# Optimization experiments

Measured on AMD Instinct MI355X. Metric: run time of the kernel, lower is better.

The kernel has to match this reference:

```python
import jax, jax.numpy as jnp
import numpy as np

B, N, CS, CV, K = 8, 2048, 256, 128, 3
EPS = 1e-6


def _eq_layernorm(s, v):
    # scalars: standard layernorm over channels; vectors: RMS of channel norms (equivariant)
    mu = s.mean(-1, keepdims=True)
    var = ((s - mu) ** 2).mean(-1, keepdims=True)
    s = (s - mu) * jax.lax.rsqrt(var + EPS)
    n2 = (v ** 2).sum(-1).mean(-1, keepdims=True)  # [b,n,1]
    v = v * jax.lax.rsqrt(n2 + EPS)[..., None]
    return s, v


def setup_inputs() -> dict:
    key = jax.random.key(0)
    ks = jax.random.split(key, 7)
    fan_s = K * (CS + CV)       # 1152
    fan_v = K * (CS + 2 * CV)   # 1536
    return {
        "x_s": jax.random.normal(ks[0], (B, N, CS), jnp.float32),
        "x_v": jax.random.normal(ks[1], (B, N, CV, 3), jnp.float32),
        "coords": jax.random.normal(ks[2], (B, N, 3), jnp.float32) * 10.0,
        "W_conv_s": jax.random.normal(ks[3], (fan_s, CS), jnp.float32),
        "W_conv_v": jax.random.normal(ks[4], (fan_v, CV), jnp.float32),
        "W_si_s": jax.random.normal(ks[5], (CS, CS), jnp.float32),
        "W_si_v": jax.random.normal(ks[6], (CV, CV), jnp.float32),
    }


def reference(x_s, x_v, coords, W_conv_s, W_conv_v, W_si_s, W_si_v):
    b, n, cs = x_s.shape
    cv = x_v.shape[2]
    pad = K // 2
    # 'same' padding: zeros for features, edge for coords (zero displacement at boundary)
    sp = jnp.pad(x_s, ((0, 0), (pad, pad), (0, 0)))
    vp = jnp.pad(x_v, ((0, 0), (pad, pad), (0, 0), (0, 0)))
    cp = jnp.pad(coords, ((0, 0), (pad, pad), (0, 0)), mode="edge")
    s_win = jnp.stack([sp[:, k:k + n] for k in range(K)], 2)   # [b,n,K,cs]
    v_win = jnp.stack([vp[:, k:k + n] for k in range(K)], 2)   # [b,n,K,cv,3]
    c_win = jnp.stack([cp[:, k:k + n] for k in range(K)], 2)   # [b,n,K,3]

    d = c_win - coords[:, :, None, :]
    dn = jnp.linalg.norm(d, axis=-1, keepdims=True)
    rhat = d * jnp.where(dn > 1e-6, 1.0 / jnp.maximum(dn, 1e-6), 0.0)

    # Clebsch-Gordan paths of (0e,1e) features with sh = (1, rhat)
    vdot = jnp.einsum("bnkcd,bnkd->bnkc", v_win, rhat)                    # 1x1 -> 0
    scal_in = jnp.concatenate([s_win, vdot], -1).reshape(b, n, -1)        # [b,n,K*(cs+cv)]
    s_rhat = s_win[..., None] * rhat[:, :, :, None, :]                    # 0x1 -> 1
    v_cross = jnp.cross(v_win, rhat[:, :, :, None, :])                    # 1x1 -> 1
    vec_in = jnp.concatenate([v_win, s_rhat, v_cross], 3).reshape(b, n, -1, 3)

    # SequenceConvolution linear mixing (fan-in normalized) + norm=True
    h_s = jnp.einsum("bnp,po->bno", scal_in, W_conv_s) / float(np.sqrt(scal_in.shape[-1]))
    h_v = jnp.einsum("bnpd,po->bnod", vec_in, W_conv_v) / float(np.sqrt(vec_in.shape[2]))
    h_s, h_v = _eq_layernorm(h_s, h_v)

    # SelfInteraction: per-degree channel mixing, residual=True, norm_last=True
    y_s = h_s + h_s @ W_si_s / float(np.sqrt(cs))
    y_v = h_v + jnp.einsum("bncd,co->bnod", h_v, W_si_v) / float(np.sqrt(cv))
    y_s, y_v = _eq_layernorm(y_s, y_v)

    # block Residual + final EquivariantLayerNorm
    z_s, z_v = _eq_layernorm(x_s + y_s, x_v + y_v)
    return z_s, z_v
```

## Files before the change

### kernel.cpp

```cpp
#include <hip/hip_runtime.h>
#include <hip/hip_bf16.h>


typedef __attribute__((ext_vector_type(8))) short short8;
typedef __attribute__((ext_vector_type(4))) short short4v;
typedef __attribute__((ext_vector_type(4))) float f32x4;
typedef unsigned short u16;

#define B_   8
#define N_   2048
#define EPS_ 1e-6f
#define TB   64

#define OFF_CS 0
#define OFF_V  294912
#define OFF_G  393216
#define OFF_SS 491520
#define OFF_SV 557056

#define MFMA(a,b,c) __builtin_amdgcn_mfma_f32_16x16x32_bf16((a),(b),(c),0,0,0)

__device__ __forceinline__ u16 f2b(float v){ __hip_bfloat16 h=__float2bfloat16(v); return *(u16*)&h; }

__global__ __launch_bounds__(256) void prep_weights(
    const float* __restrict__ Wcs, const float* __restrict__ Wcv,
    const float* __restrict__ Wss, const float* __restrict__ Wsv,
    u16* __restrict__ ws)
{
    const int bid = blockIdx.x;
    const float* src; int N, r0, ld, c0; u16* dst; int tile;
    if (bid < 288)      { src=Wcs; N=256; r0=0; dst=ws+OFF_CS; ld=1152; c0=0; tile=bid; }
    else if (bid < 336) { int k=(bid-288)/16; tile=(bid-288)%16;
                          src=Wcv; N=128; r0=k*512;     dst=ws+OFF_V; ld=768; c0=k*256; }
    else if (bid < 432) { int k=(bid-336)/32; tile=(bid-336)%32;
                          src=Wcv; N=128; r0=k*512+128; dst=ws+OFF_G; ld=768; c0=k*256; }
    else if (bid < 480) { int k=(bid-432)/16; tile=(bid-432)%16;
                          src=Wcv; N=128; r0=k*512+384; dst=ws+OFF_V; ld=768; c0=k*256+128; }
    else if (bid < 544) { tile=bid-480; src=Wss; N=256; r0=0; dst=ws+OFF_SS; ld=256; c0=0; }
    else                { tile=bid-544; src=Wsv; N=128; r0=0; dst=ws+OFF_SV; ld=128; c0=0; }
    const int ntN = N >> 5;
    const int kt = (tile/ntN)*32, nn = (tile%ntN)*32;
    __shared__ float t[32][33];
    const int r = threadIdx.x >> 5, c = threadIdx.x & 31;
#pragma unroll
    for (int i = 0; i < 4; ++i)
        t[r+8*i][c] = src[(size_t)(r0+kt+r+8*i)*N + nn+c];
    __syncthreads();
#pragma unroll
    for (int i = 0; i < 4; ++i)
        dst[(size_t)(nn+r+8*i)*ld + c0+kt+c] = f2b(t[c][r+8*i]);
}

__device__ __forceinline__ void ln_reduce(
    float p1[4][4], float p2[4][4], float pv[4][4], f32x4* red,
    int tid, int lm, int lq4, int w,
    float mu[4][4], float ss[4][4], float vs[4][4])
{
    __syncthreads();
#pragma unroll
    for (int m2 = 1; m2 < 16; m2 <<= 1)
#pragma unroll
        for (int m = 0; m < 4; ++m)
#pragma unroll
            for (int q = 0; q < 4; ++q) {
                p1[m][q] += __shfl_xor(p1[m][q], m2);
                p2[m][q] += __shfl_xor(p2[m][q], m2);
                pv[m][q] += __shfl_xor(pv[m][q], m2);
            }
    if (lm == 0)
#pragma unroll
        for (int m = 0; m < 4; ++m)
#pragma unroll
            for (int q = 0; q < 4; ++q) {
                f32x4 r = {p1[m][q], p2[m][q], pv[m][q], 0.f};
                red[(m*16+lq4+q)*8 + w] = r;
            }
    __syncthreads();
    if (tid < 64) {
        const int t = tid;
        f32x4 rs = red[t*8+0];
#pragma unroll
        for (int i = 1; i < 8; ++i) rs += red[t*8+i];
        const float mm = rs.x * (1.f/256.f);
        f32x4 fin;
        fin.x = mm;
        fin.y = rsqrtf(rs.y*(1.f/256.f) - mm*mm + EPS_);
        fin.z = rsqrtf(rs.z*(1.f/128.f) + EPS_);
        fin.w = 0.f;
        red[t*8 + (t&7)] = fin;
    }
    __syncthreads();
#pragma unroll
    for (int m = 0; m < 4; ++m)
#pragma unroll
        for (int q = 0; q < 4; ++q) {
            const int t = m*16 + lq4 + q;
            const f32x4 fin = red[t*8 + (t&7)];
            mu[m][q] = fin.x; ss[m][q] = fin.y; vs[m][q] = fin.z;
        }
}

__global__ __launch_bounds__(512, 2) void mixing_main(
    const float* __restrict__ x_s, const float* __restrict__ x_v,
    const float* __restrict__ coords, const u16* __restrict__ wt,
    float* __restrict__ out)
{
    __shared__ __align__(16) char smem[162816];
    u16*   fs  = (u16*)smem;
    u16*   fv  = (u16*)(smem + 50176);
    u16*   hsb = (u16*)smem;
    u16*   hvb = (u16*)(smem + 50176);
    float* xvL = (float*)(smem + 50176);
    float* rhp = (float*)(smem + 151552);
    f32x4* red = (f32x4*)(smem + 154624);

    const int tid = threadIdx.x;
    const int w   = tid >> 6, l = tid & 63;
    const int lm  = l & 15, lk8 = (l >> 4) << 3, lq4 = (l >> 4) << 2;
    const int gt0 = blockIdx.x * TB;
    const int n0  = gt0 & (N_ - 1);
    const int seq0 = gt0 - n0;
    const size_t ZV0 = (size_t)B_ * N_ * 256;

    if (tid < 192) {
        const int t = tid / 3, k = tid - 3 * (tid / 3);
        const int jn = n0 + t + k - 1;
        const int jc = jn < 0 ? 0 : (jn > N_-1 ? N_-1 : jn);
        const float* cj = coords + (size_t)(seq0 + jc) * 3;
        const float* c0p = coords + (size_t)(gt0 + t) * 3;
        const float d0 = cj[0]-c0p[0], d1 = cj[1]-c0p[1], d2 = cj[2]-c0p[2];
        const float dn = sqrtf(d0*d0 + d1*d1 + d2*d2);
        const float inv = dn > 1e-6f ? 1.f/dn : 0.f;
        rhp[(t*3+k)*4+0] = d0*inv; rhp[(t*3+k)*4+1] = d1*inv; rhp[(t*3+k)*4+2] = d2*inv;
    }
    __syncthreads();

    const f32x4 fz = {0.f,0.f,0.f,0.f};
    f32x4 acc_s[4][2];
    f32x4 accv[12];
#pragma unroll
    for (int m = 0; m < 4; ++m) { acc_s[m][0] = fz; acc_s[m][1] = fz; }
#pragma unroll
    for (int mi = 0; mi < 12; ++mi) accv[mi] = fz;

    const int bt = tid >> 3;
    const int bx = tid & 7;

#pragma unroll 1
    for (int k = 0; k < 3; ++k) {
        const int jn = n0 + bt + k - 1;
        const bool valid = (unsigned)jn < (unsigned)N_;
        const size_t j = (size_t)seq0 + (valid ? jn : 0);
        {
            const int c0 = bx * 32;
            const float4* sp = (const float4*)(x_s + j*256 + c0);
#pragma unroll
            for (int h = 0; h < 4; ++h) {
                float v[8];
                if (valid) {
                    const float4 f0 = sp[2*h], f1 = sp[2*h+1];
                    v[0]=f0.x; v[1]=f0.y; v[2]=f0.z; v[3]=f0.w;
                    v[4]=f1.x; v[5]=f1.y; v[6]=f1.z; v[7]=f1.w;
                } else {
#pragma unroll
                    for (int i = 0; i < 8; ++i) v[i] = 0.f;
                }
                short8 p;
#pragma unroll
                for (int i = 0; i < 8; ++i) p[i] = (short)f2b(v[i]);
                *(short8*)(fs + bt*392 + c0 + 8*h) = p;
            }
        }
        {
            const int ch0 = bx * 16;
            const float r0 = rhp[(bt*3+k)*4+0];
            const float r1 = rhp[(bt*3+k)*4+1];
            const float r2 = rhp[(bt*3+k)*4+2];
#pragma unroll
            for (int hh = 0; hh < 2; ++hh) {
                const int cb = ch0 + 8*hh;
                float vv[24];
                if (valid) {
                    const float4* vp = (const float4*)(x_v + ((size_t)j*128 + cb)*3);
#pragma unroll
                    for (int i = 0; i < 6; ++i) {
                        const float4 f = vp[i];
                        vv[4*i]=f.x; vv[4*i+1]=f.y; vv[4*i+2]=f.z; vv[4*i+3]=f.w;
                    }
                } else {
#pragma unroll
                    for (int i = 0; i < 24; ++i) vv[i] = 0.f;
                }
                short8 dv, w0, w1, w2, x0, x1, x2;
#pragma unroll
                for (int m = 0; m < 8; ++m) {
                    const float a0 = vv[3*m], a1 = vv[3*m+1], a2 = vv[3*m+2];
                    dv[m] = (short)f2b(a0*r0 + a1*r1 + a2*r2);
                    w0[m] = (short)f2b(a0); w1[m] = (short)f2b(a1); w2[m] = (short)f2b(a2);
                    x0[m] = (short)f2b(a1*r2 - a2*r1);
                    x1[m] = (short)f2b(a2*r0 - a0*r2);
                    x2[m] = (short)f2b(a0*r1 - a1*r0);
                }
                *(short8*)(fs + bt*392 + 256 + cb)            = dv;
                *(short8*)(fv + (0*64+bt)*264 + cb)           = w0;
                *(short8*)(fv + (1*64+bt)*264 + cb)           = w1;
                *(short8*)(fv + (2*64+bt)*264 + cb)           = w2;
                *(short8*)(fv + (0*64+bt)*264 + 128 + cb)     = x0;
                *(short8*)(fv + (1*64+bt)*264 + 128 + cb)     = x1;
                *(short8*)(fv + (2*64+bt)*264 + 128 + cb)     = x2;
            }
        }

        const u16* bS0 = wt + OFF_CS + k*384 + (size_t)((2*w+0)*16+lm)*1152;
        const u16* bS1 = wt + OFF_CS + k*384 + (size_t)((2*w+1)*16+lm)*1152;
        const u16* bGp = wt + OFF_G  + k*256 + (size_t)(w*16+lm)*768;
        const u16* bVp = wt + OFF_V  + k*256 + (size_t)(w*16+lm)*768;
        short8 Bs0[3], Bs1[3], Bg[3], Bv[4];
#pragma unroll
        for (int i = 0; i < 3; ++i) {
            Bs0[i] = *(const short8*)(bS0 + i*32 + lk8);
            Bs1[i] = *(const short8*)(bS1 + i*32 + lk8);
            Bg[i]  = *(const short8*)(bGp + i*32 + lk8);
        }
        __syncthreads();

        f32x4 agc[4] = {fz, fz, fz, fz};
#pragma unroll
        for (int ks = 0; ks < 12; ++ks) {
            const int r = ks % 3;
            const short8 b0 = Bs0[r], b1 = Bs1[r], bg = Bg[r];
            if (ks + 3 < 12) {
                Bs0[r] = *(const short8*)(bS0 + (ks+3)*32 + lk8);
                Bs1[r] = *(const short8*)(bS1 + (ks+3)*32 + lk8);
            }
            if (ks + 3 < 8)
                Bg[r] = *(const short8*)(bGp + (ks+3)*32 + lk8);
            if (ks == 9) {
#pragma unroll
                for (int i = 0; i < 4; ++i)
                    Bv[i] = *(const short8*)(bVp + i*32 + lk8);
            }
            const int ko = ks*32 + lk8;
#pragma unroll
            for (int m = 0; m < 4; ++m) {
                const short8 a = *(const short8*)(fs + (m*16+lm)*392 + ko);
                acc_s[m][0] = MFMA(a, b0, acc_s[m][0]);
                acc_s[m][1] = MFMA(a, b1, acc_s[m][1]);
                if (ks < 8) agc[m] = MFMA(a, bg, agc[m]);
            }
        }
#pragma unroll
        for (int ks = 0; ks < 8; ++ks) {
            const int r = ks & 3;
            const short8 bv = Bv[r];
            if (ks + 4 < 8)
                Bv[r] = *(const short8*)(bVp + (ks+4)*32 + lk8);
            const int ko = ks*32 + lk8;
#pragma unroll
            for (int mi = 0; mi < 12; ++mi) {
                const short8 a = *(const short8*)(
                    fv + ((mi>>2)*64 + (mi&3)*16 + lm)*264 + ko);
                accv[mi] = MFMA(a, bv, accv[mi]);
            }
        }
#pragma unroll
        for (int mi = 0; mi < 12; ++mi) {
            const int m = mi & 3, d = mi >> 2;
#pragma unroll
            for (int q = 0; q < 4; ++q)
                accv[mi][q] += agc[m][q] * rhp[((m*16+lq4+q)*3 + k)*4 + d];
        }
        __syncthreads();
    }

    const float inv_fs = 0.029462783f;
    const float inv_fv = 0.0255155136f;
#pragma unroll
    for (int m = 0; m < 4; ++m)
#pragma unroll
        for (int u = 0; u < 2; ++u)
#pragma unroll
            for (int q = 0; q < 4; ++q) acc_s[m][u][q] *= inv_fs;
#pragma unroll
    for (int mi = 0; mi < 12; ++mi)
#pragma unroll
        for (int q = 0; q < 4; ++q) accv[mi][q] *= inv_fv;

    float p1[4][4], p2[4][4], pv[4][4], mu[4][4], ss[4][4], vs[4][4];
#pragma unroll
    for (int m = 0; m < 4; ++m)
#pragma unroll
        for (int q = 0; q < 4; ++q) {
            float a = 0.f, b = 0.f, c = 0.f;
#pragma unroll
            for (int u = 0; u < 2; ++u) { const float x = acc_s[m][u][q]; a += x; b += x*x; }
#pragma unroll
            for (int d = 0; d < 3; ++d) { const float x = accv[d*4+m][q]; c += x*x; }
            p1[m][q] = a; p2[m][q] = b; pv[m][q] = c;
        }
    ln_reduce(p1, p2, pv, red, tid, lm, lq4, w, mu, ss, vs);

#pragma unroll
    for (int m = 0; m < 4; ++m)
#pragma unroll
        for (int u = 0; u < 2; ++u)
#pragma unroll
            for (int q = 0; q < 4; ++q) {
                const float h = (acc_s[m][u][q] - mu[m][q]) * ss[m][q];
                acc_s[m][u][q] = h;
                hsb[(m*16+lq4+q)*264 + (2*w+u)*16 + lm] = f2b(h);
            }
#pragma unroll
    for (int mi = 0; mi < 12; ++mi)
#pragma unroll
        for (int q = 0; q < 4; ++q) {
            const float h = accv[mi][q] * vs[mi&3][q];
            accv[mi][q] = h;
            hvb[((mi>>2)*64 + (mi&3)*16 + lq4 + q)*136 + w*16 + lm] = f2b(h);
        }

    const u16* bP0 = wt + OFF_SS + (size_t)((2*w+0)*16+lm)*256;
    const u16* bP1 = wt + OFF_SS + (size_t)((2*w+1)*16+lm)*256;
    const u16* bPv = wt + OFF_SV + (size_t)(w*16+lm)*128;
    short8 Cs0[3], Cs1[3], Cv[4];
#pragma unroll
    for (int i = 0; i < 3; ++i) {
        Cs0[i] = *(const short8*)(bP0 + i*32 + lk8);
        Cs1[i] = *(const short8*)(bP1 + i*32 + lk8);
    }
#pragma unroll
    for (int i = 0; i < 4; ++i)
        Cv[i] = *(const short8*)(bPv + i*32 + lk8);
    __syncthreads();

    f32x4 accs[4][2];
    f32x4 accw[12];
#pragma unroll
    for (int m = 0; m < 4; ++m) { accs[m][0] = fz; accs[m][1] = fz; }
#pragma unroll
    for (int mi = 0; mi < 12; ++mi) accw[mi] = fz;
#pragma unroll
    for (int ks = 0; ks < 8; ++ks) {
        const int r = ks % 3;
        const short8 c0 = Cs0[r], c1 = Cs1[r];
        if (ks + 3 < 8) {
            Cs0[r] = *(const short8*)(bP0 + (ks+3)*32 + lk8);
            Cs1[r] = *(const short8*)(bP1 + (ks+3)*32 + lk8);
        }
        const int ko = ks*32 + lk8;
#pragma unroll
        for (int m = 0; m < 4; ++m) {
            const short8 a = *(const short8*)(hsb + (m*16+lm)*264 + ko);
            accs[m][0] = MFMA(a, c0, accs[m][0]);
            accs[m][1] = MFMA(a, c1, accs[m][1]);
        }
    }
#pragma unroll
    for (int ks = 0; ks < 4; ++ks) {
        const int ko = ks*32 + lk8;
#pragma unroll
        for (int mi = 0; mi < 12; ++mi) {
            const short8 a = *(const short8*)(
                hvb + ((mi>>2)*64 + (mi&3)*16 + lm)*136 + ko);
            accw[mi] = MFMA(a, Cv[ks], accw[mi]);
        }
    }

#pragma unroll
    for (int m = 0; m < 4; ++m)
#pragma unroll
        for (int u = 0; u < 2; ++u)
#pragma unroll
            for (int q = 0; q < 4; ++q) acc_s[m][u][q] += accs[m][u][q] * 0.0625f;
#pragma unroll
    for (int mi = 0; mi < 12; ++mi)
#pragma unroll
        for (int q = 0; q < 4; ++q) accv[mi][q] += accw[mi][q] * 0.08838834764f;

#pragma unroll
    for (int m = 0; m < 4; ++m)
#pragma unroll
        for (int q = 0; q < 4; ++q) {
            float a = 0.f, b = 0.f, c = 0.f;
#pragma unroll
            for (int u = 0; u < 2; ++u) { const float x = acc_s[m][u][q]; a += x; b += x*x; }
#pragma unroll
            for (int d = 0; d < 3; ++d) { const float x = accv[d*4+m][q]; c += x*x; }
            p1[m][q] = a; p2[m][q] = b; pv[m][q] = c;
        }
    float4 xr[12];
    {
        const float4* xvsrc = (const float4*)(x_v + (size_t)gt0 * 384);
#pragma unroll
        for (int i = 0; i < 12; ++i) xr[i] = xvsrc[tid + i*512];
    }
    ln_reduce(p1, p2, pv, red, tid, lm, lq4, w, mu, ss, vs);
#pragma unroll
    for (int i = 0; i < 12; ++i) {
        const int e4 = tid + i*512;
        const int t = e4 / 96, c4 = e4 - t*96;
        *(float4*)(xvL + t*388 + c4*4) = xr[i];
    }
    __syncthreads();

#pragma unroll
    for (int m = 0; m < 4; ++m)
#pragma unroll
        for (int u = 0; u < 2; ++u)
#pragma unroll
            for (int q = 0; q < 4; ++q)
                acc_s[m][u][q] = (acc_s[m][u][q] - mu[m][q]) * ss[m][q]
                    + x_s[(size_t)(gt0 + m*16 + lq4 + q)*256 + (2*w+u)*16 + lm];
#pragma unroll
    for (int mi = 0; mi < 12; ++mi)
#pragma unroll
        for (int q = 0; q < 4; ++q) {
            const int t = (mi&3)*16 + lq4 + q;
            accv[mi][q] = accv[mi][q] * vs[mi&3][q]
                + xvL[t*388 + (w*16+lm)*3 + (mi>>2)];
        }

#pragma unroll
    for (int m = 0; m < 4; ++m)
#pragma unroll
        for (int q = 0; q < 4; ++q) {
            float a = 0.f, b = 0.f, c = 0.f;
#pragma unroll
            for (int u = 0; u < 2; ++u) { const float x = acc_s[m][u][q]; a += x; b += x*x; }
#pragma unroll
            for (int d = 0; d < 3; ++d) { const float x = accv[d*4+m][q]; c += x*x; }
            p1[m][q] = a; p2[m][q] = b; pv[m][q] = c;
        }
    ln_reduce(p1, p2, pv, red, tid, lm, lq4, w, mu, ss, vs);

#pragma unroll
    for (int m = 0; m < 4; ++m)
#pragma unroll
        for (int u = 0; u < 2; ++u)
#pragma unroll
            for (int q = 0; q < 4; ++q)
                out[(size_t)(gt0 + m*16 + lq4 + q)*256 + (2*w+u)*16 + lm] =
                    (acc_s[m][u][q] - mu[m][q]) * ss[m][q];
#pragma unroll
    for (int mi = 0; mi < 12; ++mi)
#pragma unroll
        for (int q = 0; q < 4; ++q) {
            const int t = (mi&3)*16 + lq4 + q;
            xvL[t*388 + (w*16+lm)*3 + (mi>>2)] = accv[mi][q] * vs[mi&3][q];
        }
    __syncthreads();
    {
        f32x4* dst = (f32x4*)(out + ZV0 + (size_t)gt0 * 384);
#pragma unroll
        for (int i = 0; i < 12; ++i) {
            const int e4 = tid + i*512;
            const int t = e4 / 96, c4 = e4 - t*96;
            const f32x4 v = *(const f32x4*)(xvL + t*388 + c4*4);
            __builtin_nontemporal_store(v, dst + e4);
        }
    }
}

extern "C" void kernel_launch(void* const* d_in, const int* in_sizes, int n_in,
                              void* d_out, int out_size, void* d_ws, size_t ws_size,
                              hipStream_t stream) {
    const float* x_s    = (const float*)d_in[0];
    const float* x_v    = (const float*)d_in[1];
    const float* coords = (const float*)d_in[2];
    const float* Wcs    = (const float*)d_in[3];
    const float* Wcv    = (const float*)d_in[4];
    const float* Wss    = (const float*)d_in[5];
    const float* Wsv    = (const float*)d_in[6];
    float* out = (float*)d_out;
    u16* ws = (u16*)d_ws;

    hipLaunchKernelGGL(prep_weights, dim3(560), dim3(256), 0, stream,
                       Wcs, Wcv, Wss, Wsv, ws);
    hipLaunchKernelGGL(mixing_main, dim3((B_ * N_) / TB), dim3(512), 0, stream,
                       x_s, x_v, coords, ws, out);
}
```

Before: 101.2 us.

## Retile vector-path MFMA work as 2x2 warp tiles over tokens and channels

```diff
diff --git a/kernel.cpp b/kernel.cpp
--- a/kernel.cpp
+++ b/kernel.cpp
@@ -3,7 +3,6 @@
 
 
 typedef __attribute__((ext_vector_type(8))) short short8;
-typedef __attribute__((ext_vector_type(4))) short short4v;
 typedef __attribute__((ext_vector_type(4))) float f32x4;
 typedef unsigned short u16;
 
@@ -117,6 +116,8 @@
     const int tid = threadIdx.x;
     const int w   = tid >> 6, l = tid & 63;
     const int lm  = l & 15, lk8 = (l >> 4) << 3, lq4 = (l >> 4) << 2;
+    const int wh2 = w & 3;
+    const int th  = w >> 2;
     const int gt0 = blockIdx.x * TB;
     const int n0  = gt0 & (N_ - 1);
     const int seq0 = gt0 - n0;
@@ -137,11 +138,13 @@
 
     const f32x4 fz = {0.f,0.f,0.f,0.f};
     f32x4 acc_s[4][2];
-    f32x4 accv[12];
+    f32x4 accv[3][2][2];
 #pragma unroll
     for (int m = 0; m < 4; ++m) { acc_s[m][0] = fz; acc_s[m][1] = fz; }
 #pragma unroll
-    for (int mi = 0; mi < 12; ++mi) accv[mi] = fz;
+    for (int d = 0; d < 3; ++d)
+#pragma unroll
+        for (int tf = 0; tf < 2; ++tf) { accv[d][tf][0] = fz; accv[d][tf][1] = fz; }
 
     const int bt = tid >> 3;
     const int bx = tid & 7;
@@ -213,63 +216,82 @@
 
         const u16* bS0 = wt + OFF_CS + k*384 + (size_t)((2*w+0)*16+lm)*1152;
         const u16* bS1 = wt + OFF_CS + k*384 + (size_t)((2*w+1)*16+lm)*1152;
-        const u16* bGp = wt + OFF_G  + k*256 + (size_t)(w*16+lm)*768;
-        const u16* bVp = wt + OFF_V  + k*256 + (size_t)(w*16+lm)*768;
-        short8 Bs0[3], Bs1[3], Bg[3], Bv[4];
+        const u16* bG0 = wt + OFF_G  + k*256 + (size_t)((2*wh2+0)*16+lm)*768;
+        const u16* bG1 = wt + OFF_G  + k*256 + (size_t)((2*wh2+1)*16+lm)*768;
+        const u16* bV0 = wt + OFF_V  + k*256 + (size_t)((2*wh2+0)*16+lm)*768;
+        const u16* bV1 = wt + OFF_V  + k*256 + (size_t)((2*wh2+1)*16+lm)*768;
+        short8 Bs0[3], Bs1[3];
 #pragma unroll
         for (int i = 0; i < 3; ++i) {
             Bs0[i] = *(const short8*)(bS0 + i*32 + lk8);
             Bs1[i] = *(const short8*)(bS1 + i*32 + lk8);
-            Bg[i]  = *(const short8*)(bGp + i*32 + lk8);
         }
         __syncthreads();
 
-        f32x4 agc[4] = {fz, fz, fz, fz};
+        f32x4 agc[2][2] = {{fz,fz},{fz,fz}};
 #pragma unroll
         for (int ks = 0; ks < 12; ++ks) {
             const int r = ks % 3;
-            const short8 b0 = Bs0[r], b1 = Bs1[r], bg = Bg[r];
+            const short8 b0 = Bs0[r], b1 = Bs1[r];
             if (ks + 3 < 12) {
                 Bs0[r] = *(const short8*)(bS0 + (ks+3)*32 + lk8);
                 Bs1[r] = *(const short8*)(bS1 + (ks+3)*32 + lk8);
             }
-            if (ks + 3 < 8)
-                Bg[r] = *(const short8*)(bGp + (ks+3)*32 + lk8);
-            if (ks == 9) {
-#pragma unroll
-                for (int i = 0; i < 4; ++i)
-                    Bv[i] = *(const short8*)(bVp + i*32 + lk8);
-            }
             const int ko = ks*32 + lk8;
-#pragma unroll
-            for (int m = 0; m < 4; ++m) {
-                const short8 a = *(const short8*)(fs + (m*16+lm)*392 + ko);
-                acc_s[m][0] = MFMA(a, b0, acc_s[m][0]);
-                acc_s[m][1] = MFMA(a, b1, acc_s[m][1]);
-                if (ks < 8) agc[m] = MFMA(a, bg, agc[m]);
+            const short8 a0 = *(const short8*)(fs + ( 0+lm)*392 + ko);
+            const short8 a1 = *(const short8*)(fs + (16+lm)*392 + ko);
+            const short8 a2 = *(const short8*)(fs + (32+lm)*392 + ko);
+            const short8 a3 = *(const short8*)(fs + (48+lm)*392 + ko);
+            acc_s[0][0] = MFMA(a0, b0, acc_s[0][0]);
+            acc_s[0][1] = MFMA(a0, b1, acc_s[0][1]);
+            acc_s[1][0] = MFMA(a1, b0, acc_s[1][0]);
+            acc_s[1][1] = MFMA(a1, b1, acc_s[1][1]);
+            acc_s[2][0] = MFMA(a2, b0, acc_s[2][0]);
+            acc_s[2][1] = MFMA(a2, b1, acc_s[2][1]);
+            acc_s[3][0] = MFMA(a3, b0, acc_s[3][0]);
+            acc_s[3][1] = MFMA(a3, b1, acc_s[3][1]);
+            if (ks < 8) {
+                const short8 g0 = *(const short8*)(bG0 + ko);
+                const short8 g1 = *(const short8*)(bG1 + ko);
+                if (th == 0) {
+                    agc[0][0] = MFMA(a0, g0, agc[0][0]);
+                    agc[0][1] = MFMA(a0, g1, agc[0][1]);
+                    agc[1][0] = MFMA(a1, g0, agc[1][0]);
+                    agc[1][1] = MFMA(a1, g1, agc[1][1]);
+                } else {
+                    agc[0][0] = MFMA(a2, g0, agc[0][0]);
+                    agc[0][1] = MFMA(a2, g1, agc[0][1]);
+                    agc[1][0] = MFMA(a3, g0, agc[1][0]);
+                    agc[1][1] = MFMA(a3, g1, agc[1][1]);
+                }
             }
         }
 #pragma unroll
         for (int ks = 0; ks < 8; ++ks) {
-            const int r = ks & 3;
-            const short8 bv = Bv[r];
-            if (ks + 4 < 8)
-                Bv[r] = *(const short8*)(bVp + (ks+4)*32 + lk8);
             const int ko = ks*32 + lk8;
-#pragma unroll
-            for (int mi = 0; mi < 12; ++mi) {
-                const short8 a = *(const short8*)(
-                    fv + ((mi>>2)*64 + (mi&3)*16 + lm)*264 + ko);
-                accv[mi] = MFMA(a, bv, accv[mi]);
-            }
-        }
-#pragma unroll
-        for (int mi = 0; mi < 12; ++mi) {
-            const int m = mi & 3, d = mi >> 2;
-#pragma unroll
-            for (int q = 0; q < 4; ++q)
-                accv[mi][q] += agc[m][q] * rhp[((m*16+lq4+q)*3 + k)*4 + d];
-        }
+            const short8 bv0 = *(const short8*)(bV0 + ko);
+            const short8 bv1 = *(const short8*)(bV1 + ko);
+#pragma unroll
+            for (int d = 0; d < 3; ++d)
+#pragma unroll
+                for (int tf = 0; tf < 2; ++tf) {
+                    const short8 a = *(const short8*)(
+                        fv + (d*64 + (2*th+tf)*16 + lm)*264 + ko);
+                    accv[d][tf][0] = MFMA(a, bv0, accv[d][tf][0]);
+                    accv[d][tf][1] = MFMA(a, bv1, accv[d][tf][1]);
+                }
+        }
+#pragma unroll
+        for (int d = 0; d < 3; ++d)
+#pragma unroll
+            for (int tf = 0; tf < 2; ++tf)
+#pragma unroll
+                for (int u2 = 0; u2 < 2; ++u2)
+#pragma unroll
+                    for (int q = 0; q < 4; ++q) {
+                        const int t = (2*th+tf)*16 + lq4 + q;
+                        accv[d][tf][u2][q] += agc[tf][u2][q] * rhp[(t*3+k)*4+d];
+                    }
         __syncthreads();
     }
 
@@ -282,23 +304,41 @@
 #pragma unroll
             for (int q = 0; q < 4; ++q) acc_s[m][u][q] *= inv_fs;
 #pragma unroll
-    for (int mi = 0; mi < 12; ++mi)
-#pragma unroll
-        for (int q = 0; q < 4; ++q) accv[mi][q] *= inv_fv;
+    for (int d = 0; d < 3; ++d)
+#pragma unroll
+        for (int tf = 0; tf < 2; ++tf)
+#pragma unroll
+            for (int u2 = 0; u2 < 2; ++u2)
+#pragma unroll
+                for (int q = 0; q < 4; ++q) accv[d][tf][u2][q] *= inv_fv;
 
     float p1[4][4], p2[4][4], pv[4][4], mu[4][4], ss[4][4], vs[4][4];
-#pragma unroll
-    for (int m = 0; m < 4; ++m)
-#pragma unroll
-        for (int q = 0; q < 4; ++q) {
-            float a = 0.f, b = 0.f, c = 0.f;
+    float vstA[4], vstB[4];
+#pragma unroll
+    for (int q = 0; q < 4; ++q) {
+        float cA = 0.f, cB = 0.f;
+#pragma unroll
+        for (int d = 0; d < 3; ++d)
+#pragma unroll
+            for (int u2 = 0; u2 < 2; ++u2) {
+                const float xa = accv[d][0][u2][q]; cA += xa*xa;
+                const float xb = accv[d][1][u2][q]; cB += xb*xb;
+            }
+#pragma unroll
+        for (int m = 0; m < 4; ++m) {
+            float a = 0.f, b = 0.f;
 #pragma unroll
             for (int u = 0; u < 2; ++u) { const float x = acc_s[m][u][q]; a += x; b += x*x; }
-#pragma unroll
-            for (int d = 0; d < 3; ++d) { const float x = accv[d*4+m][q]; c += x*x; }
-            p1[m][q] = a; p2[m][q] = b; pv[m][q] = c;
-        }
+            p1[m][q] = a; p2[m][q] = b;
+            pv[m][q] = (m == 2*th) ? cA : ((m == 2*th+1) ? cB : 0.f);
+        }
+    }
     ln_reduce(p1, p2, pv, red, tid, lm, lq4, w, mu, ss, vs);
+#pragma unroll
+    for (int q = 0; q < 4; ++q) {
+        vstA[q] = th ? vs[2][q] : vs[0][q];
+        vstB[q] = th ? vs[3][q] : vs[1][q];
+    }
 
 #pragma unroll
     for (int m = 0; m < 4; ++m)
@@ -311,34 +351,38 @@
                 hsb[(m*16+lq4+q)*264 + (2*w+u)*16 + lm] = f2b(h);
             }
 #pragma unroll
-    for (int mi = 0; mi < 12; ++mi)
-#pragma unroll
-        for (int q = 0; q < 4; ++q) {
-            const float h = accv[mi][q] * vs[mi&3][q];
-            accv[mi][q] = h;
-            hvb[((mi>>2)*64 + (mi&3)*16 + lq4 + q)*136 + w*16 + lm] = f2b(h);
-        }
+    for (int d = 0; d < 3; ++d)
+#pragma unroll
+        for (int tf = 0; tf < 2; ++tf)
+#pragma unroll
+            for (int u2 = 0; u2 < 2; ++u2)
+#pragma unroll
+                for (int q = 0; q < 4; ++q) {
+                    const float h = accv[d][tf][u2][q] * (tf ? vstB[q] : vstA[q]);
+                    accv[d][tf][u2][q] = h;
+                    hvb[(d*64 + (2*th+tf)*16 + lq4 + q)*136 + (2*wh2+u2)*16 + lm] = f2b(h);
+                }
 
     const u16* bP0 = wt + OFF_SS + (size_t)((2*w+0)*16+lm)*256;
     const u16* bP1 = wt + OFF_SS + (size_t)((2*w+1)*16+lm)*256;
-    const u16* bPv = wt + OFF_SV + (size_t)(w*16+lm)*128;
-    short8 Cs0[3], Cs1[3], Cv[4];
+    const u16* cQ0 = wt + OFF_SV + (size_t)((2*wh2+0)*16+lm)*128;
+    const u16* cQ1 = wt + OFF_SV + (size_t)((2*wh2+1)*16+lm)*128;
+    short8 Cs0[3], Cs1[3];
 #pragma unroll
     for (int i = 0; i < 3; ++i) {
         Cs0[i] = *(const short8*)(bP0 + i*32 + lk8);
         Cs1[i] = *(const short8*)(bP1 + i*32 + lk8);
     }
-#pragma unroll
-    for (int i = 0; i < 4; ++i)
-        Cv[i] = *(const short8*)(bPv + i*32 + lk8);
     __syncthreads();
 
     f32x4 accs[4][2];
-    f32x4 accw[12];
+    f32x4 accw[3][2][2];
 #pragma unroll
     for (int m = 0; m < 4; ++m) { accs[m][0] = fz; accs[m][1] = fz; }
 #pragma unroll
-    for (int mi = 0; mi < 12; ++mi) accw[mi] = fz;
+    for (int d = 0; d < 3; ++d)
+#pragma unroll
+        for (int tf = 0; tf < 2; ++tf) { accw[d][tf][0] = fz; accw[d][tf][1] = fz; }
 #pragma unroll
     for (int ks = 0; ks < 8; ++ks) {
         const int r = ks % 3;
@@ -358,12 +402,17 @@
 #pragma unroll
     for (int ks = 0; ks < 4; ++ks) {
         const int ko = ks*32 + lk8;
-#pragma unroll
-        for (int mi = 0; mi < 12; ++mi) {
-            const short8 a = *(const short8*)(
-                hvb + ((mi>>2)*64 + (mi&3)*16 + lm)*136 + ko);
-            accw[mi] = MFMA(a, Cv[ks], accw[mi]);
-        }
+        const short8 c0 = *(const short8*)(cQ0 + ko);
+        const short8 c1 = *(const short8*)(cQ1 + ko);
+#pragma unroll
+        for (int d = 0; d < 3; ++d)
+#pragma unroll
+            for (int tf = 0; tf < 2; ++tf) {
+                const short8 a = *(const short8*)(
+                    hvb + (d*64 + (2*th+tf)*16 + lm)*136 + ko);
+                accw[d][tf][0] = MFMA(a, c0, accw[d][tf][0]);
+                accw[d][tf][1] = MFMA(a, c1, accw[d][tf][1]);
+            }
     }
 
 #pragma unroll
@@ -373,21 +422,34 @@
 #pragma unroll
             for (int q = 0; q < 4; ++q) acc_s[m][u][q] += accs[m][u][q] * 0.0625f;
 #pragma unroll
-    for (int mi = 0; mi < 12; ++mi)
-#pragma unroll
-        for (int q = 0; q < 4; ++q) accv[mi][q] += accw[mi][q] * 0.08838834764f;
-
-#pragma unroll
-    for (int m = 0; m < 4; ++m)
-#pragma unroll
-        for (int q = 0; q < 4; ++q) {
-            float a = 0.f, b = 0.f, c = 0.f;
+    for (int d = 0; d < 3; ++d)
+#pragma unroll
+        for (int tf = 0; tf < 2; ++tf)
+#pragma unroll
+            for (int u2 = 0; u2 < 2; ++u2)
+#pragma unroll
+                for (int q = 0; q < 4; ++q)
+                    accv[d][tf][u2][q] += accw[d][tf][u2][q] * 0.08838834764f;
+
+#pragma unroll
+    for (int q = 0; q < 4; ++q) {
+        float cA = 0.f, cB = 0.f;
+#pragma unroll
+        for (int d = 0; d < 3; ++d)
+#pragma unroll
+            for (int u2 = 0; u2 < 2; ++u2) {
+                const float xa = accv[d][0][u2][q]; cA += xa*xa;
+                const float xb = accv[d][1][u2][q]; cB += xb*xb;
+            }
+#pragma unroll
+        for (int m = 0; m < 4; ++m) {
+            float a = 0.f, b = 0.f;
 #pragma unroll
             for (int u = 0; u < 2; ++u) { const float x = acc_s[m][u][q]; a += x; b += x*x; }
-#pragma unroll
-            for (int d = 0; d < 3; ++d) { const float x = accv[d*4+m][q]; c += x*x; }
-            p1[m][q] = a; p2[m][q] = b; pv[m][q] = c;
-        }
+            p1[m][q] = a; p2[m][q] = b;
+            pv[m][q] = (m == 2*th) ? cA : ((m == 2*th+1) ? cB : 0.f);
+        }
+    }
     float4 xr[12];
     {
         const float4* xvsrc = (const float4*)(x_v + (size_t)gt0 * 384);
@@ -395,6 +457,11 @@
         for (int i = 0; i < 12; ++i) xr[i] = xvsrc[tid + i*512];
     }
     ln_reduce(p1, p2, pv, red, tid, lm, lq4, w, mu, ss, vs);
+#pragma unroll
+    for (int q = 0; q < 4; ++q) {
+        vstA[q] = th ? vs[2][q] : vs[0][q];
+        vstB[q] = th ? vs[3][q] : vs[1][q];
+    }
 #pragma unroll
     for (int i = 0; i < 12; ++i) {
         const int e4 = tid + i*512;
@@ -412,26 +479,43 @@
                 acc_s[m][u][q] = (acc_s[m][u][q] - mu[m][q]) * ss[m][q]
                     + x_s[(size_t)(gt0 + m*16 + lq4 + q)*256 + (2*w+u)*16 + lm];
 #pragma unroll
-    for (int mi = 0; mi < 12; ++mi)
-#pragma unroll
-        for (int q = 0; q < 4; ++q) {
-            const int t = (mi&3)*16 + lq4 + q;
-            accv[mi][q] = accv[mi][q] * vs[mi&3][q]
-                + xvL[t*388 + (w*16+lm)*3 + (mi>>2)];
-        }
-
-#pragma unroll
-    for (int m = 0; m < 4; ++m)
-#pragma unroll
-        for (int q = 0; q < 4; ++q) {
-            float a = 0.f, b = 0.f, c = 0.f;
+    for (int d = 0; d < 3; ++d)
+#pragma unroll
+        for (int tf = 0; tf < 2; ++tf)
+#pragma unroll
+            for (int u2 = 0; u2 < 2; ++u2)
+#pragma unroll
+                for (int q = 0; q < 4; ++q) {
+                    const int t = (2*th+tf)*16 + lq4 + q;
+                    accv[d][tf][u2][q] = accv[d][tf][u2][q] * (tf ? vstB[q] : vstA[q])
+                        + xvL[t*388 + ((2*wh2+u2)*16 + lm)*3 + d];
+                }
+
+#pragma unroll
+    for (int q = 0; q < 4; ++q) {
+        float cA = 0.f, cB = 0.f;
+#pragma unroll
+        for (int d = 0; d < 3; ++d)
+#pragma unroll
+            for (int u2 = 0; u2 < 2; ++u2) {
+                const float xa = accv[d][0][u2][q]; cA += xa*xa;
+                const float xb = accv[d][1][u2][q]; cB += xb*xb;
+            }
+#pragma unroll
+        for (int m = 0; m < 4; ++m) {
+            float a = 0.f, b = 0.f;
 #pragma unroll
             for (int u = 0; u < 2; ++u) { const float x = acc_s[m][u][q]; a += x; b += x*x; }
-#pragma unroll
-            for (int d = 0; d < 3; ++d) { const float x = accv[d*4+m][q]; c += x*x; }
-            p1[m][q] = a; p2[m][q] = b; pv[m][q] = c;
-        }
+            p1[m][q] = a; p2[m][q] = b;
+            pv[m][q] = (m == 2*th) ? cA : ((m == 2*th+1) ? cB : 0.f);
+        }
+    }
     ln_reduce(p1, p2, pv, red, tid, lm, lq4, w, mu, ss, vs);
+#pragma unroll
+    for (int q = 0; q < 4; ++q) {
+        vstA[q] = th ? vs[2][q] : vs[0][q];
+        vstB[q] = th ? vs[3][q] : vs[1][q];
+    }
 
 #pragma unroll
     for (int m = 0; m < 4; ++m)
@@ -442,12 +526,17 @@
                 out[(size_t)(gt0 + m*16 + lq4 + q)*256 + (2*w+u)*16 + lm] =
                     (acc_s[m][u][q] - mu[m][q]) * ss[m][q];
 #pragma unroll
-    for (int mi = 0; mi < 12; ++mi)
-#pragma unroll
-        for (int q = 0; q < 4; ++q) {
-            const int t = (mi&3)*16 + lq4 + q;
-            xvL[t*388 + (w*16+lm)*3 + (mi>>2)] = accv[mi][q] * vs[mi&3][q];
-        }
+    for (int d = 0; d < 3; ++d)
+#pragma unroll
+        for (int tf = 0; tf < 2; ++tf)
+#pragma unroll
+            for (int u2 = 0; u2 < 2; ++u2)
+#pragma unroll
+                for (int q = 0; q < 4; ++q) {
+                    const int t = (2*th+tf)*16 + lq4 + q;
+                    xvL[t*388 + ((2*wh2+u2)*16 + lm)*3 + d] =
+                        accv[d][tf][u2][q] * (tf ? vstB[q] : vstA[q]);
+                }
     __syncthreads();
     {
         f32x4* dst = (f32x4*)(out + ZV0 + (size_t)gt0 * 384);
```

Measured after the change: 106.3 us. 1.05x slower.
